# Kernel tuning notes

Hardware: AMD Instinct MI355X
Metric: run time of the kernel (lower is better)

The kernel has to match this reference:

```python
import jax, jax.numpy as jnp
import numpy as np

N_ENT = 100000
N_USR = 30000
N_TOT = N_ENT + N_USR
N_REL = 32
D = 64
E = 500000
INTER = 500000
N_LAYERS = 2
SLOPE = 0.01  # torch nn.LeakyReLU default negative slope


def _seg_softmax(logits, seg, n):
    # sparse softmax over rows (segments)
    m = jax.ops.segment_max(logits, seg, num_segments=n)
    ex = jnp.exp(logits - m[seg])
    den = jax.ops.segment_sum(ex, seg, num_segments=n)
    return ex / den[seg]


def setup_inputs() -> dict:
    key = jax.random.key(0)
    k = jax.random.split(key, 14)
    all_embed = jax.random.normal(k[0], (N_TOT, D), jnp.float32) * 0.1
    rel_embed = jax.random.normal(k[1], (N_REL, D), jnp.float32) * 0.1
    Wk_w = jax.random.normal(k[2], (D, 2 * D), jnp.float32) / np.sqrt(2 * D)
    Wk_b = jnp.zeros((D,), jnp.float32)
    Wa_w = jax.random.normal(k[3], (D, D), jnp.float32) / np.sqrt(D)
    Wb_w = jax.random.normal(k[4], (D, D), jnp.float32) / np.sqrt(D)
    # KG edge lists (head entity, tail entity, relation)
    h_list = jnp.sort(jax.random.randint(k[5], (E,), 0, N_ENT))
    t_list = jax.random.randint(k[6], (E,), 0, N_ENT)
    r_list = jax.random.randint(k[7], (E,), 0, N_REL)
    # bipartite interaction matrix A_in (symmetric, items rows first then users)
    u = jax.random.randint(k[8], (INTER,), 0, N_USR)
    it = jax.random.randint(k[9], (INTER,), 0, N_ENT)
    a_row = jnp.concatenate([it, N_ENT + u])
    a_col = jnp.concatenate([N_ENT + u, it])
    a_vals = jax.random.uniform(k[10], (2 * INTER,), jnp.float32) * 0.01
    # calc_score ids: user ids are offset by n_entities in the concatenated table
    user_ids = N_ENT + jax.random.randint(k[11], (1024,), 0, N_USR)
    item_ids = jax.random.randint(k[12], (2048,), 0, N_ENT)
    return dict(all_embed=all_embed, rel_embed=rel_embed, Wk_w=Wk_w, Wk_b=Wk_b,
                Wa_w=Wa_w, Wb_w=Wb_w, a_vals=a_vals, user_ids=user_ids,
                item_ids=item_ids, h_list=h_list, t_list=t_list, r_list=r_list,
                a_row=a_row, a_col=a_col)


def _get_embeddings(all_embed, rel_embed, Wk_w, Wk_b, Wa_w, Wb_w, a_vals,
                    h_list, t_list, r_list, a_row, a_col):
    e_ent = all_embed[:N_ENT]
    e_usr = all_embed[N_ENT:]
    user_list = [e_usr]
    item_list = [e_ent]
    e_items_dual = e_ent
    e_users_curr = e_usr
    e_ent_curr = e_ent
    r_e = rel_embed[r_list]  # (E, D) -- constant across layers
    for _ in range(N_LAYERS):
        # --- KG attention (Eq. 2): gather + concat + linear + dot + leakyrelu ---
        h_e = e_ent_curr[h_list]            # (E, D)
        t_e = e_ent_curr[t_list]            # (E, D)
        cat = jnp.concatenate([t_e, h_e], axis=1)   # (E, 2D)
        trans = cat @ Wk_w.T + Wk_b                 # (E, D)
        logits = jnp.sum(trans * r_e, axis=1)       # (E,)
        vals = jnp.where(logits >= 0, logits, SLOPE * logits)
        alpha = _seg_softmax(vals, h_list, N_ENT)   # row-wise sparse softmax
        # --- KG aggregation (Eq. 1): spmm ---
        e_items_kg = jax.ops.segment_sum(alpha[:, None] * t_e, h_list,
                                         num_segments=N_ENT)
        # --- IG aggregation (Eq. 3 & 6): spmm with A_in ---
        ig_in = jnp.concatenate([e_items_dual, e_users_curr], axis=0)  # (N_TOT, D)
        ig_out = jax.ops.segment_sum(a_vals[:, None] * ig_in[a_col], a_row,
                                     num_segments=N_TOT)
        e_items_collab = ig_out[:N_ENT]
        e_users_new = ig_out[N_ENT:]
        # --- fusion gate (Eq. 4, 5) ---
        g = jax.nn.sigmoid(e_items_kg @ Wa_w.T + e_items_collab @ Wb_w.T)
        e_items_dual = g * e_items_kg + (1.0 - g) * e_items_collab
        item_list.append(e_items_collab)
        user_list.append(e_users_new)
        e_users_curr = e_users_new
        e_ent_curr = e_items_kg
    item_final = sum(item_list)
    user_final = sum(user_list)
    return jnp.concatenate([item_final, user_final], axis=0)


def reference(all_embed, rel_embed, Wk_w, Wk_b, Wa_w, Wb_w, a_vals,
              user_ids, item_ids, h_list, t_list, r_list, a_row, a_col):
    all_final = _get_embeddings(all_embed, rel_embed, Wk_w, Wk_b, Wa_w, Wb_w,
                                a_vals, h_list, t_list, r_list, a_row, a_col)
    user_e = all_final[user_ids]   # (Bu, D)
    item_e = all_final[item_ids]   # (Bi, D)
    return user_e @ item_e.T       # (Bu, Bi)
```

## Files before the change

kernel.cpp:

```cpp
#include <hip/hip_runtime.h>
#include <hip/hip_bf16.h>

#define N_ENT 100000
#define N_USR 30000
#define N_TOTN 130000
#define N_RELC 32
#define DIM 64
#define NEDGE 500000
#define INTER 500000
#define SLOPE 0.01f
#define CPT_NB 127
#define FILL_NB 1954
#define ATT_NB 1024
#define RSTR 64

typedef unsigned char u8;
typedef unsigned long long u64;

__device__ __forceinline__ float grp_sum16(float v){
  v += __shfl_xor(v, 8, 64);
  v += __shfl_xor(v, 4, 64);
  v += __shfl_xor(v, 2, 64);
  v += __shfl_xor(v, 1, 64);
  return v;
}

__global__ void __launch_bounds__(256) k_prep(
    const float* __restrict__ rel, const float* __restrict__ Wk,
    const float* __restrict__ Wkb, float* __restrict__ m, float* __restrict__ b,
    const int* __restrict__ user_ids, const int* __restrict__ item_ids,
    u8* __restrict__ r2_item, u8* __restrict__ r2_user){
  int bid = blockIdx.x;
  if (bid < 17){
    int idx = bid*256 + threadIdx.x;
    if (idx < N_RELC*128){
      int r = idx >> 7, j = idx & 127;
      float s = 0.f;
      for (int d = 0; d < DIM; ++d) s += rel[r*DIM+d] * Wk[d*128+j];
      m[idx] = s;
    } else if (idx < N_RELC*128 + N_RELC){
      int r = idx - N_RELC*128;
      float s = 0.f;
      for (int d = 0; d < DIM; ++d) s += Wkb[d] * rel[r*DIM+d];
      b[r] = s;
    }
  } else {
    int i = (bid - 17)*256 + threadIdx.x;
    if (i < 1024) r2_user[user_ids[i] - N_ENT] = 1;
    else if (i < 3072) r2_item[item_ids[i - 1024]] = 1;
  }
}

__global__ void k_mark(const int* __restrict__ a_row, const int* __restrict__ a_col,
                       const u8* __restrict__ r2_item, const u8* __restrict__ r2_user,
                       u8* __restrict__ need_d, u8* __restrict__ need_u){
  int i = blockIdx.x*256 + threadIdx.x;
  if (i >= INTER) return;
  int it = a_row[i];
  int uu = a_col[i] - N_ENT;
  if (r2_item[it]) need_u[uu] = 1;
  if (r2_user[uu]) need_d[it] = 1;
}

__global__ void __launch_bounds__(256) k_buildfill(
    const int* __restrict__ a_row, const int* __restrict__ a_col,
    const float* __restrict__ a_vals,
    const u8* __restrict__ need_d, const u8* __restrict__ need_u,
    const u8* __restrict__ r2_item, const u8* __restrict__ r2_user,
    int* __restrict__ list_gate, int* __restrict__ list_s1,
    int* __restrict__ counters, int* __restrict__ cnt, int2* __restrict__ csr){
  if (blockIdx.x < CPT_NB){
    __shared__ u64 mg_sh[16], ms_sh[16];
    __shared__ int pre_g[16], pre_s[16];
    __shared__ int base_sh[2];
    int t = threadIdx.x;
    int wave = t >> 6, lane = t & 63;
    bool pg[4], ps[4];
    int ibase = blockIdx.x*1024;
    #pragma unroll
    for (int k = 0; k < 4; ++k){
      int i = ibase + k*256 + t;
      bool g = false, s = false;
      if (i < N_TOTN){
        if (i < N_ENT){ g = need_d[i] != 0; s = g || (r2_item[i] != 0); }
        else { int u = i - N_ENT; s = (need_u[u] != 0) || (r2_user[u] != 0); }
      }
      pg[k] = g; ps[k] = s;
      u64 mg = __ballot(g), ms = __ballot(s);
      if (lane == 0){ mg_sh[k*4 + wave] = mg; ms_sh[k*4 + wave] = ms; }
    }
    __syncthreads();
    if (t == 0){
      int sg = 0, ss = 0;
      for (int j = 0; j < 16; ++j){
        pre_g[j] = sg; sg += __popcll(mg_sh[j]);
        pre_s[j] = ss; ss += __popcll(ms_sh[j]);
      }
      base_sh[0] = sg ? atomicAdd(&counters[0], sg) : 0;
      base_sh[1] = ss ? atomicAdd(&counters[1], ss) : 0;
    }
    __syncthreads();
    int bg = base_sh[0], bs = base_sh[1];
    u64 lmask = (1ull << lane) - 1;
    #pragma unroll
    for (int k = 0; k < 4; ++k){
      int i = ibase + k*256 + t;
      if (pg[k]) list_gate[bg + pre_g[k*4+wave] + __popcll(mg_sh[k*4+wave] & lmask)] = i;
      if (ps[k]) list_s1 [bs + pre_s[k*4+wave] + __popcll(ms_sh[k*4+wave] & lmask)] = i;
    }
  } else {
    int i = (blockIdx.x - CPT_NB)*256 + threadIdx.x;
    if (i >= INTER) return;
    int it = a_row[i];
    int uc = a_col[i];
    int uu = uc - N_ENT;
    if (need_d[it] | r2_item[it]){
      int p = atomicAdd(&cnt[it], 1);
      if (p < RSTR) csr[((size_t)it << 6) + p] = make_int2(uc, __float_as_int(a_vals[i]));
    }
    if (need_u[uu] | r2_user[uu]){
      int p = atomicAdd(&cnt[uc], 1);
      if (p < RSTR) csr[((size_t)uc << 6) + p] = make_int2(it, __float_as_int(a_vals[i + INTER]));
    }
  }
}

__global__ void __launch_bounds__(256) k_l1(const float4* __restrict__ ent4,
    const float4* __restrict__ m4, const float* __restrict__ bvec,
    const int* __restrict__ h_list, const int* __restrict__ t_list,
    const int* __restrict__ r_list, const int* __restrict__ list_gate,
    const int* __restrict__ list_s1, const int* __restrict__ counters,
    float4* __restrict__ kg4, const int* __restrict__ cnt,
    const int2* __restrict__ csr,
    float4* __restrict__ collab4, float4* __restrict__ x2_4){
  if (blockIdx.x < ATT_NB){
    __shared__ float4 msh[N_RELC*32];
    __shared__ float bsh[N_RELC];
    for (int i = threadIdx.x; i < N_RELC*32; i += 256) msh[i] = m4[i];
    if (threadIdx.x < N_RELC) bsh[threadIdx.x] = bvec[threadIdx.x];
    __syncthreads();
    int n = counters[0];
    int sub = threadIdx.x & 15;
    int grp = (blockIdx.x*256 + threadIdx.x) >> 4;
    int ng = (ATT_NB*256) >> 4;
    for (int idx = grp; idx < n; idx += ng){
      int s = list_gate[idx];
      int lo = 0, hi = NEDGE;
      while (lo < hi){ int mid = (lo + hi) >> 1; if (h_list[mid] < s) lo = mid + 1; else hi = mid; }
      int beg = lo;
      hi = NEDGE;
      while (lo < hi){ int mid = (lo + hi) >> 1; if (h_list[mid] <= s) lo = mid + 1; else hi = mid; }
      int end = lo;
      float4 h4 = ent4[(size_t)s*16 + sub];
      float l = 0.f;
      float4 acc = {0.f,0.f,0.f,0.f};
      for (int base = beg; base < end; base += 16){
        int mch = end - base; if (mch > 16) mch = 16;
        int tj = 0, rj = 0;
        if (sub < mch){ tj = t_list[base + sub]; rj = r_list[base + sub]; }
        #pragma unroll 4
        for (int j = 0; j < mch; ++j){
          int ti = __shfl(tj, j, 16);
          int r  = __shfl(rj, j, 16);
          float4 t4 = ent4[(size_t)ti*16 + sub];
          float4 mt = msh[r*32 + sub];
          float4 mh = msh[r*32 + 16 + sub];
          float v = t4.x*mt.x + t4.y*mt.y + t4.z*mt.z + t4.w*mt.w
                  + h4.x*mh.x + h4.y*mh.y + h4.z*mh.z + h4.w*mh.w;
          v = grp_sum16(v) + bsh[r];
          v = (v >= 0.f) ? v : SLOPE * v;
          float w = __expf(v);
          l += w;
          acc.x += w*t4.x; acc.y += w*t4.y; acc.z += w*t4.z; acc.w += w*t4.w;
        }
      }
      float inv = (end > beg) ? 1.f / l : 0.f;
      float4 o = {acc.x*inv, acc.y*inv, acc.z*inv, acc.w*inv};
      kg4[(size_t)s*16 + sub] = o;
    }
  } else {
    int n = counters[1];
    int sub = threadIdx.x & 15;
    int bid = blockIdx.x - ATT_NB;
    int nb = gridDim.x - ATT_NB;
    int grp = (bid*256 + threadIdx.x) >> 4;
    int ng = (nb*256) >> 4;
    for (int idx = grp; idx < n; idx += ng){
      int i = list_s1[idx];
      int deg = cnt[i]; if (deg > RSTR) deg = RSTR;
      size_t base0 = (size_t)i << 6;
      float4 acc = {0.f,0.f,0.f,0.f};
      for (int b = 0; b < deg; b += 16){
        int mch = deg - b; if (mch > 16) mch = 16;
        int2 e = make_int2(0, 0);
        if (sub < mch) e = csr[base0 + b + sub];
        #pragma unroll 4
        for (int j = 0; j < mch; ++j){
          int cj = __shfl(e.x, j, 16);
          float vj = __int_as_float(__shfl(e.y, j, 16));
          float4 sv = ent4[(size_t)cj*16 + sub];
          acc.x += vj*sv.x; acc.y += vj*sv.y; acc.z += vj*sv.z; acc.w += vj*sv.w;
        }
      }
      if (i < N_ENT) collab4[(size_t)i*16 + sub] = acc;
      else x2_4[(size_t)i*16 + sub] = acc;
    }
  }
}

__global__ void __launch_bounds__(256) k_gate(const float* __restrict__ kg,
    const float* __restrict__ collab, const float* __restrict__ Wa,
    const float* __restrict__ Wb, float* __restrict__ x2dual,
    const int* __restrict__ list, const int* __restrict__ counters){
  int n = counters[0];
  int row0 = blockIdx.x * 64;
  if (row0 >= n) return;
  __shared__ float Xsh[64][129];
  __shared__ float Wsh[128][65];
  for (int i = threadIdx.x; i < 64*64; i += 256){
    int a = i >> 6, j = i & 63;
    Wsh[j][a] = Wa[i];
    Wsh[64 + j][a] = Wb[i];
  }
  for (int i = threadIdx.x; i < 64*128; i += 256){
    int r = i >> 7, c = i & 127;
    int idx = row0 + r;
    float v = 0.f;
    if (idx < n){
      int row = list[idx];
      v = (c < 64) ? kg[(size_t)row*64 + c] : collab[(size_t)row*64 + (c - 64)];
    }
    Xsh[r][c] = v;
  }
  __syncthreads();
  int ct = threadIdx.x & 15, rt = threadIdx.x >> 4;
  int r0 = rt * 4, c0 = ct * 4;
  float acc[4][4] = {};
  for (int k = 0; k < 128; ++k){
    float w0 = Wsh[k][c0], w1 = Wsh[k][c0+1], w2 = Wsh[k][c0+2], w3 = Wsh[k][c0+3];
    #pragma unroll
    for (int i = 0; i < 4; ++i){
      float x = Xsh[r0+i][k];
      acc[i][0] += x*w0; acc[i][1] += x*w1; acc[i][2] += x*w2; acc[i][3] += x*w3;
    }
  }
  #pragma unroll
  for (int i = 0; i < 4; ++i){
    int idx = row0 + r0 + i;
    if (idx < n){
      int row = list[idx];
      float4 o;
      #pragma unroll
      for (int j = 0; j < 4; ++j){
        int c = c0 + j;
        float g = 1.f / (1.f + __expf(-acc[i][j]));
        float kv = Xsh[r0+i][c];
        float cv = Xsh[r0+i][64 + c];
        (&o.x)[j] = g*kv + (1.f - g)*cv;
      }
      *(float4*)&x2dual[(size_t)row*64 + c0] = o;
    }
  }
}

__global__ void __launch_bounds__(256) k_spmm2g(const int* __restrict__ cnt,
    const int2* __restrict__ csr, const float* __restrict__ x2,
    const float* __restrict__ all_embed, const float* __restrict__ collab1,
    const int* __restrict__ user_ids, const int* __restrict__ item_ids,
    float* __restrict__ user_e, float* __restrict__ item_e){
  int lane = threadIdx.x & 63;
  int g = (blockIdx.x*256 + threadIdx.x) >> 6;
  if (g >= 3072) return;
  int id;
  float b1;
  if (g < 1024){
    id = user_ids[g];
    b1 = x2[(size_t)id*64 + lane];
  } else {
    id = item_ids[g - 1024];
    b1 = collab1[(size_t)id*64 + lane];
  }
  float acc = all_embed[(size_t)id*64 + lane] + b1;
  int deg = cnt[id]; if (deg > RSTR) deg = RSTR;
  size_t base0 = (size_t)id << 6;
  int2 e = make_int2(0, 0);
  if (lane < deg) e = csr[base0 + lane];
  for (int j = 0; j < deg; ++j){
    int cj = __shfl(e.x, j, 64);
    float vj = __int_as_float(__shfl(e.y, j, 64));
    acc += vj * x2[(size_t)cj*64 + lane];
  }
  if (g < 1024) user_e[(size_t)g*64 + lane] = acc;
  else item_e[(size_t)(g - 1024)*64 + lane] = acc;
}

__global__ void __launch_bounds__(256) k_out(const float* __restrict__ ue,
    const float* __restrict__ ie, float* __restrict__ out){
  __shared__ float ash[64][65];
  __shared__ float bsh[64][65];
  int row0 = blockIdx.y * 64, col0 = blockIdx.x * 64;
  for (int i = threadIdx.x; i < 64*64; i += 256){
    int r = i >> 6, c = i & 63;
    ash[r][c] = ue[(size_t)(row0 + r)*DIM + c];
    bsh[r][c] = ie[(size_t)(col0 + r)*DIM + c];
  }
  __syncthreads();
  int tx = threadIdx.x & 15, ty = threadIdx.x >> 4;
  int r0 = ty*4, c0 = tx*4;
  float acc[4][4] = {};
  #pragma unroll
  for (int k = 0; k < 64; ++k){
    float a0 = ash[r0][k], a1 = ash[r0+1][k], a2 = ash[r0+2][k], a3 = ash[r0+3][k];
    float b0 = bsh[c0][k], b1 = bsh[c0+1][k], b2 = bsh[c0+2][k], b3 = bsh[c0+3][k];
    acc[0][0] += a0*b0; acc[0][1] += a0*b1; acc[0][2] += a0*b2; acc[0][3] += a0*b3;
    acc[1][0] += a1*b0; acc[1][1] += a1*b1; acc[1][2] += a1*b2; acc[1][3] += a1*b3;
    acc[2][0] += a2*b0; acc[2][1] += a2*b1; acc[2][2] += a2*b2; acc[2][3] += a2*b3;
    acc[3][0] += a3*b0; acc[3][1] += a3*b1; acc[3][2] += a3*b2; acc[3][3] += a3*b3;
  }
  #pragma unroll
  for (int i = 0; i < 4; ++i){
    float4 o = {acc[i][0], acc[i][1], acc[i][2], acc[i][3]};
    *(float4*)&out[(size_t)(row0 + r0 + i)*2048 + col0 + c0] = o;
  }
}

extern "C" void kernel_launch(void* const* d_in, const int* in_sizes, int n_in,
                              void* d_out, int out_size, void* d_ws, size_t ws_size,
                              hipStream_t stream){
  const float* all_embed = (const float*)d_in[0];
  const float* rel_embed = (const float*)d_in[1];
  const float* Wk_w      = (const float*)d_in[2];
  const float* Wk_b      = (const float*)d_in[3];
  const float* Wa_w      = (const float*)d_in[4];
  const float* Wb_w      = (const float*)d_in[5];
  const float* a_vals    = (const float*)d_in[6];
  const int* user_ids   = (const int*)d_in[7];
  const int* item_ids   = (const int*)d_in[8];
  const int* h_list     = (const int*)d_in[9];
  const int* t_list     = (const int*)d_in[10];
  const int* r_list     = (const int*)d_in[11];
  const int* a_row      = (const int*)d_in[12];
  const int* a_col      = (const int*)d_in[13];
  float* out = (float*)d_out;

  char* p = (char*)d_ws;
  auto alloc = [&](size_t bytes)->void*{
    void* r = (void*)p;
    p += (bytes + 255) & ~(size_t)255;
    return r;
  };
  float* m_rel   = (float*)alloc((size_t)N_RELC*128*4);
  float* b_rel   = (float*)alloc((size_t)N_RELC*4);
  size_t zbytes = (size_t)N_TOTN*4 + 256 + (2*(size_t)N_ENT + 2*(size_t)N_USR);
  char*  zbase  = (char*)alloc(zbytes);
  int*   cnt      = (int*)zbase;
  int*   counters = (int*)(zbase + (size_t)N_TOTN*4);
  u8*    r2_item  = (u8*)(zbase + (size_t)N_TOTN*4 + 256);
  u8*    r2_user  = r2_item + N_ENT;
  u8*    need_d   = r2_user + N_USR;
  u8*    need_u   = need_d + N_ENT;
  int2*  csr     = (int2*) alloc((size_t)N_TOTN*RSTR*8);
  int*   list_gate = (int*)alloc((size_t)N_ENT*4);
  int*   list_s1   = (int*)alloc((size_t)N_TOTN*4);
  float* kg1     = (float*)alloc((size_t)N_ENT*DIM*4);
  float* collab1 = (float*)alloc((size_t)N_ENT*DIM*4);
  float* x2      = (float*)alloc((size_t)N_TOTN*DIM*4);
  float* user_e  = (float*)alloc((size_t)1024*DIM*4);
  float* item_e  = (float*)alloc((size_t)2048*DIM*4);

  hipMemsetAsync(zbase, 0, zbytes, stream);
  k_prep<<<29, 256, 0, stream>>>(rel_embed, Wk_w, Wk_b, m_rel, b_rel,
      user_ids, item_ids, r2_item, r2_user);
  k_mark<<<(INTER + 255)/256, 256, 0, stream>>>(a_row, a_col, r2_item, r2_user, need_d, need_u);
  k_buildfill<<<CPT_NB + FILL_NB, 256, 0, stream>>>(a_row, a_col, a_vals,
      need_d, need_u, r2_item, r2_user, list_gate, list_s1, counters, cnt, csr);

  k_l1<<<ATT_NB + 2048, 256, 0, stream>>>((const float4*)all_embed,
      (const float4*)m_rel, b_rel, h_list, t_list, r_list, list_gate, list_s1,
      counters, (float4*)kg1, cnt, csr, (float4*)collab1, (float4*)x2);
  k_gate<<<(N_ENT + 63)/64, 256, 0, stream>>>(kg1, collab1, Wa_w, Wb_w, x2,
      list_gate, counters);
  k_spmm2g<<<768, 256, 0, stream>>>(cnt, csr, x2, all_embed, collab1,
      user_ids, item_ids, user_e, item_e);
  dim3 grid_out(2048/64, 1024/64);
  k_out<<<grid_out, 256, 0, stream>>>(user_e, item_e, out);
}
```

Baseline: 208.4 us.

## Precompute KG head offsets, vectorize mark/fill loads, persist gate blocks

Builds a CSR-style offset array over the sorted head list inside the prep kernel, so the attention kernel reads row bounds directly instead of running two binary searches per entity. The mark and fill kernels now load four edges per thread with int4/float4 loads, and the gate kernel becomes a grid-stride loop over 256 blocks so the weight tile is staged into shared memory once per block rather than once per 64 rows. A small unroll pragma is added to the second-layer SpMM loop. The offset fill adds extra prep blocks, and the per-thread fill loop can be uneven when head ids have gaps.

```diff
diff --git a/kernel.cpp b/kernel.cpp
--- a/kernel.cpp
+++ b/kernel.cpp
@@ -10,9 +10,11 @@
 #define INTER 500000
 #define SLOPE 0.01f
 #define CPT_NB 127
-#define FILL_NB 1954
+#define FILL_NB 489
+#define MARK_NB 489
 #define ATT_NB 1024
 #define RSTR 64
+#define KGOFF_NB 1954
 
 typedef unsigned char u8;
 typedef unsigned long long u64;
@@ -29,7 +31,8 @@
     const float* __restrict__ rel, const float* __restrict__ Wk,
     const float* __restrict__ Wkb, float* __restrict__ m, float* __restrict__ b,
     const int* __restrict__ user_ids, const int* __restrict__ item_ids,
-    u8* __restrict__ r2_item, u8* __restrict__ r2_user){
+    u8* __restrict__ r2_item, u8* __restrict__ r2_user,
+    const int* __restrict__ h_list, int* __restrict__ off){
   int bid = blockIdx.x;
   if (bid < 17){
     int idx = bid*256 + threadIdx.x;
@@ -44,22 +47,34 @@
       for (int d = 0; d < DIM; ++d) s += Wkb[d] * rel[r*DIM+d];
       b[r] = s;
     }
-  } else {
+  } else if (bid < 29){
     int i = (bid - 17)*256 + threadIdx.x;
     if (i < 1024) r2_user[user_ids[i] - N_ENT] = 1;
     else if (i < 3072) r2_item[item_ids[i - 1024]] = 1;
-  }
-}
-
-__global__ void k_mark(const int* __restrict__ a_row, const int* __restrict__ a_col,
+  } else {
+    int e = (bid - 29)*256 + threadIdx.x;
+    if (e <= NEDGE){
+      int hc = (e < NEDGE) ? h_list[e] : N_ENT;
+      int hp = (e == 0) ? -1 : h_list[e-1];
+      for (int s = hp+1; s <= hc; ++s) off[s] = e;
+    }
+  }
+}
+
+__global__ void k_mark(const int4* __restrict__ a_row4, const int4* __restrict__ a_col4,
                        const u8* __restrict__ r2_item, const u8* __restrict__ r2_user,
                        u8* __restrict__ need_d, u8* __restrict__ need_u){
   int i = blockIdx.x*256 + threadIdx.x;
-  if (i >= INTER) return;
-  int it = a_row[i];
-  int uu = a_col[i] - N_ENT;
-  if (r2_item[it]) need_u[uu] = 1;
-  if (r2_user[uu]) need_d[it] = 1;
+  if (i >= INTER/4) return;
+  int4 ar = a_row4[i];
+  int4 ac = a_col4[i];
+  #pragma unroll
+  for (int k = 0; k < 4; ++k){
+    int it = (&ar.x)[k];
+    int uu = (&ac.x)[k] - N_ENT;
+    if (r2_item[it]) need_u[uu] = 1;
+    if (r2_user[uu]) need_d[it] = 1;
+  }
 }
 
 __global__ void __launch_bounds__(256) k_buildfill(
@@ -110,24 +125,31 @@
     }
   } else {
     int i = (blockIdx.x - CPT_NB)*256 + threadIdx.x;
-    if (i >= INTER) return;
-    int it = a_row[i];
-    int uc = a_col[i];
-    int uu = uc - N_ENT;
-    if (need_d[it] | r2_item[it]){
-      int p = atomicAdd(&cnt[it], 1);
-      if (p < RSTR) csr[((size_t)it << 6) + p] = make_int2(uc, __float_as_int(a_vals[i]));
-    }
-    if (need_u[uu] | r2_user[uu]){
-      int p = atomicAdd(&cnt[uc], 1);
-      if (p < RSTR) csr[((size_t)uc << 6) + p] = make_int2(it, __float_as_int(a_vals[i + INTER]));
+    if (i >= INTER/4) return;
+    int4 ar = ((const int4*)a_row)[i];
+    int4 ac = ((const int4*)a_col)[i];
+    float4 av0 = ((const float4*)a_vals)[i];
+    float4 av1 = ((const float4*)(a_vals + INTER))[i];
+    #pragma unroll
+    for (int k = 0; k < 4; ++k){
+      int it = (&ar.x)[k];
+      int uc = (&ac.x)[k];
+      int uu = uc - N_ENT;
+      if (need_d[it] | r2_item[it]){
+        int p = atomicAdd(&cnt[it], 1);
+        if (p < RSTR) csr[((size_t)it << 6) + p] = make_int2(uc, __float_as_int((&av0.x)[k]));
+      }
+      if (need_u[uu] | r2_user[uu]){
+        int p = atomicAdd(&cnt[uc], 1);
+        if (p < RSTR) csr[((size_t)uc << 6) + p] = make_int2(it, __float_as_int((&av1.x)[k]));
+      }
     }
   }
 }
 
 __global__ void __launch_bounds__(256) k_l1(const float4* __restrict__ ent4,
     const float4* __restrict__ m4, const float* __restrict__ bvec,
-    const int* __restrict__ h_list, const int* __restrict__ t_list,
+    const int* __restrict__ off, const int* __restrict__ t_list,
     const int* __restrict__ r_list, const int* __restrict__ list_gate,
     const int* __restrict__ list_s1, const int* __restrict__ counters,
     float4* __restrict__ kg4, const int* __restrict__ cnt,
@@ -145,12 +167,7 @@
     int ng = (ATT_NB*256) >> 4;
     for (int idx = grp; idx < n; idx += ng){
       int s = list_gate[idx];
-      int lo = 0, hi = NEDGE;
-      while (lo < hi){ int mid = (lo + hi) >> 1; if (h_list[mid] < s) lo = mid + 1; else hi = mid; }
-      int beg = lo;
-      hi = NEDGE;
-      while (lo < hi){ int mid = (lo + hi) >> 1; if (h_list[mid] <= s) lo = mid + 1; else hi = mid; }
-      int end = lo;
+      int beg = off[s], end = off[s+1];
       float4 h4 = ent4[(size_t)s*16 + sub];
       float l = 0.f;
       float4 acc = {0.f,0.f,0.f,0.f};
@@ -213,8 +230,6 @@
     const float* __restrict__ Wb, float* __restrict__ x2dual,
     const int* __restrict__ list, const int* __restrict__ counters){
   int n = counters[0];
-  int row0 = blockIdx.x * 64;
-  if (row0 >= n) return;
   __shared__ float Xsh[64][129];
   __shared__ float Wsh[128][65];
   for (int i = threadIdx.x; i < 64*64; i += 256){
@@ -222,43 +237,46 @@
     Wsh[j][a] = Wa[i];
     Wsh[64 + j][a] = Wb[i];
   }
-  for (int i = threadIdx.x; i < 64*128; i += 256){
-    int r = i >> 7, c = i & 127;
-    int idx = row0 + r;
-    float v = 0.f;
-    if (idx < n){
-      int row = list[idx];
-      v = (c < 64) ? kg[(size_t)row*64 + c] : collab[(size_t)row*64 + (c - 64)];
-    }
-    Xsh[r][c] = v;
-  }
-  __syncthreads();
   int ct = threadIdx.x & 15, rt = threadIdx.x >> 4;
   int r0 = rt * 4, c0 = ct * 4;
-  float acc[4][4] = {};
-  for (int k = 0; k < 128; ++k){
-    float w0 = Wsh[k][c0], w1 = Wsh[k][c0+1], w2 = Wsh[k][c0+2], w3 = Wsh[k][c0+3];
+  for (int row0 = blockIdx.x*64; row0 < n; row0 += gridDim.x*64){
+    __syncthreads();
+    for (int i = threadIdx.x; i < 64*128; i += 256){
+      int r = i >> 7, c = i & 127;
+      int idx = row0 + r;
+      float v = 0.f;
+      if (idx < n){
+        int row = list[idx];
+        v = (c < 64) ? kg[(size_t)row*64 + c] : collab[(size_t)row*64 + (c - 64)];
+      }
+      Xsh[r][c] = v;
+    }
+    __syncthreads();
+    float acc[4][4] = {};
+    for (int k = 0; k < 128; ++k){
+      float w0 = Wsh[k][c0], w1 = Wsh[k][c0+1], w2 = Wsh[k][c0+2], w3 = Wsh[k][c0+3];
+      #pragma unroll
+      for (int i = 0; i < 4; ++i){
+        float x = Xsh[r0+i][k];
+        acc[i][0] += x*w0; acc[i][1] += x*w1; acc[i][2] += x*w2; acc[i][3] += x*w3;
+      }
+    }
     #pragma unroll
     for (int i = 0; i < 4; ++i){
-      float x = Xsh[r0+i][k];
-      acc[i][0] += x*w0; acc[i][1] += x*w1; acc[i][2] += x*w2; acc[i][3] += x*w3;
-    }
-  }
-  #pragma unroll
-  for (int i = 0; i < 4; ++i){
-    int idx = row0 + r0 + i;
-    if (idx < n){
-      int row = list[idx];
-      float4 o;
-      #pragma unroll
-      for (int j = 0; j < 4; ++j){
-        int c = c0 + j;
-        float g = 1.f / (1.f + __expf(-acc[i][j]));
-        float kv = Xsh[r0+i][c];
-        float cv = Xsh[r0+i][64 + c];
-        (&o.x)[j] = g*kv + (1.f - g)*cv;
-      }
-      *(float4*)&x2dual[(size_t)row*64 + c0] = o;
+      int idx = row0 + r0 + i;
+      if (idx < n){
+        int row = list[idx];
+        float4 o;
+        #pragma unroll
+        for (int j = 0; j < 4; ++j){
+          int c = c0 + j;
+          float g = 1.f / (1.f + __expf(-acc[i][j]));
+          float kv = Xsh[r0+i][c];
+          float cv = Xsh[r0+i][64 + c];
+          (&o.x)[j] = g*kv + (1.f - g)*cv;
+        }
+        *(float4*)&x2dual[(size_t)row*64 + c0] = o;
+      }
     }
   }
 }
@@ -285,6 +303,7 @@
   size_t base0 = (size_t)id << 6;
   int2 e = make_int2(0, 0);
   if (lane < deg) e = csr[base0 + lane];
+  #pragma unroll 4
   for (int j = 0; j < deg; ++j){
     int cj = __shfl(e.x, j, 64);
     float vj = __int_as_float(__shfl(e.y, j, 64));
@@ -351,6 +370,7 @@
   };
   float* m_rel   = (float*)alloc((size_t)N_RELC*128*4);
   float* b_rel   = (float*)alloc((size_t)N_RELC*4);
+  int*   kg_off  = (int*)  alloc((size_t)(N_ENT+1)*4);
   size_t zbytes = (size_t)N_TOTN*4 + 256 + (2*(size_t)N_ENT + 2*(size_t)N_USR);
   char*  zbase  = (char*)alloc(zbytes);
   int*   cnt      = (int*)zbase;
@@ -369,16 +389,17 @@
   float* item_e  = (float*)alloc((size_t)2048*DIM*4);
 
   hipMemsetAsync(zbase, 0, zbytes, stream);
-  k_prep<<<29, 256, 0, stream>>>(rel_embed, Wk_w, Wk_b, m_rel, b_rel,
-      user_ids, item_ids, r2_item, r2_user);
-  k_mark<<<(INTER + 255)/256, 256, 0, stream>>>(a_row, a_col, r2_item, r2_user, need_d, need_u);
+  k_prep<<<29 + KGOFF_NB, 256, 0, stream>>>(rel_embed, Wk_w, Wk_b,
+      m_rel, b_rel, user_ids, item_ids, r2_item, r2_user, h_list, kg_off);
+  k_mark<<<MARK_NB, 256, 0, stream>>>((const int4*)a_row, (const int4*)a_col,
+      r2_item, r2_user, need_d, need_u);
   k_buildfill<<<CPT_NB + FILL_NB, 256, 0, stream>>>(a_row, a_col, a_vals,
       need_d, need_u, r2_item, r2_user, list_gate, list_s1, counters, cnt, csr);
 
   k_l1<<<ATT_NB + 2048, 256, 0, stream>>>((const float4*)all_embed,
-      (const float4*)m_rel, b_rel, h_list, t_list, r_list, list_gate, list_s1,
+      (const float4*)m_rel, b_rel, kg_off, t_list, r_list, list_gate, list_s1,
       counters, (float4*)kg1, cnt, csr, (float4*)collab1, (float4*)x2);
-  k_gate<<<(N_ENT + 63)/64, 256, 0, stream>>>(kg1, collab1, Wa_w, Wb_w, x2,
+  k_gate<<<256, 256, 0, stream>>>(kg1, collab1, Wa_w, Wb_w, x2,
       list_gate, counters);
   k_spmm2g<<<768, 256, 0, stream>>>(cnt, csr, x2, all_embed, collab1,
       user_ids, item_ids, user_e, item_e);
```

After: 201.3 us. -3.4%, faster.
